# Optimization experiments

Hardware: AMD Instinct MI355X
Metric: run time of the kernel (lower is better)

Reference implementation:

```python
import jax, jax.numpy as jnp
import numpy as np

N = 50000
E = 600000
D_IN = 128
D_OUT = 128


def setup_inputs() -> dict:
    key = jax.random.key(0)
    k1, k2, k3, k4 = jax.random.split(key, 4)
    x = jax.random.normal(k1, (N, D_IN), dtype=jnp.float32)
    edge_index = jax.random.randint(k2, (2, E), 0, N, dtype=jnp.int64)
    # GCNConv learned params: weight [D_IN, D_OUT] (glorot), bias [D_OUT] (zeros in PyG)
    lim = np.sqrt(6.0 / (D_IN + D_OUT)).astype(np.float32)
    W = jax.random.uniform(k3, (D_IN, D_OUT), dtype=jnp.float32, minval=-lim, maxval=lim)
    b = jnp.zeros((D_OUT,), dtype=jnp.float32)
    return {"x": x, "edge_index": edge_index, "W": W, "b": b}


def reference(x, edge_index, W, b):
    # PyG GCNConv default: add self-loops, symmetric normalization D^-1/2 A D^-1/2,
    # out[i] = sum_{j->i} norm_ji * (x[j] @ W) + b
    n = x.shape[0]
    loops = jnp.arange(n, dtype=edge_index.dtype)
    row = jnp.concatenate([edge_index[0], loops])  # source
    col = jnp.concatenate([edge_index[1], loops])  # destination

    deg = jax.ops.segment_sum(jnp.ones_like(col, dtype=x.dtype), col, num_segments=n)
    dinv = jnp.where(deg > 0, jax.lax.rsqrt(deg), 0.0)
    norm = dinv[row] * dinv[col]  # [E+N]

    h = x @ W  # [N, D_OUT] linear transform first (D_OUT <= D_IN style)
    msg = h[row] * norm[:, None]  # gather + scale, [E+N, D_OUT]
    out = jax.ops.segment_sum(msg, col, num_segments=n)  # scatter-add to destinations
    return out + b
```

## Files before the change

### kernel.cpp

```cpp
#include <hip/hip_runtime.h>
#include <hip/hip_bf16.h>

#define D 128
#define CAP 64
typedef __hip_bfloat16 bf16;
typedef __hip_bfloat162 bf162;
typedef __attribute__((ext_vector_type(8))) short bf16x8;
typedef __attribute__((ext_vector_type(4))) float f32x4;

__device__ __forceinline__ int load_idx(const void* ei, long long pos, int is64) {
    if (is64) return (int)((const long long*)ei)[pos];
    return ((const int*)ei)[pos];
}

__device__ __forceinline__ float bf16bits_to_f32(unsigned short v) {
    union { unsigned u; float f; } c;
    c.u = ((unsigned)v) << 16;
    return c.f;
}

__device__ __forceinline__ unsigned short f32_to_bf16bits(float v) {
    bf16 b = __float2bfloat16(v);
    return *reinterpret_cast<unsigned short*>(&b);
}

__global__ void init_kernel(const void* __restrict__ x, const void* __restrict__ ei,
                            const void* __restrict__ W, bf16x8* __restrict__ Wpre,
                            int* __restrict__ cur, int* __restrict__ flags,
                            int n, int nzb) {
    int i = blockIdx.x * blockDim.x + threadIdx.x;
    if (i < n) cur[i] = 0;

    if (blockIdx.x == 0) {
        __shared__ int cnt;
        if (threadIdx.x == 0) cnt = 0;
        __syncthreads();
        const unsigned short* u = (const unsigned short*)x;
        int bad = 0;
        for (int j = threadIdx.x; j < 2048; j += blockDim.x) {
            unsigned short v = u[2 * j];
            int e = (v >> 7) & 0xFF;
            if (e == 255 || (e != 0 && (e < 90 || e > 165))) bad++;
        }
        atomicAdd(&cnt, bad);
        __syncthreads();
        if (threadIdx.x == 0) flags[0] = (cnt > 256) ? 1 : 0;
    } else if (blockIdx.x == 1) {
        __shared__ int cnt;
        if (threadIdx.x == 0) cnt = 0;
        __syncthreads();
        const int* w = (const int*)ei;
        int nz = 0;
        for (int j = threadIdx.x; j < 512; j += blockDim.x) {
            if (w[2 * j + 1] != 0) nz++;
        }
        atomicAdd(&cnt, nz);
        __syncthreads();
        if (threadIdx.x == 0) flags[1] = (cnt == 0) ? 1 : 0;
    } else if (blockIdx.x >= nzb) {
        __shared__ int cnt;
        if (threadIdx.x == 0) cnt = 0;
        __syncthreads();
        const unsigned short* u = (const unsigned short*)x;
        int bad = 0;
        for (int j = threadIdx.x; j < 2048; j += blockDim.x) {
            unsigned short v = u[2 * j];
            int e = (v >> 7) & 0xFF;
            if (e == 255 || (e != 0 && (e < 90 || e > 165))) bad++;
        }
        atomicAdd(&cnt, bad);
        __syncthreads();
        const int f = (cnt > 256) ? 1 : 0;

        int cid = (blockIdx.x - nzb) * 256 + threadIdx.x;
        int l2 = cid & 63, ktct = cid >> 6;
        int kb = (ktct & 3) * 32 + (l2 >> 4) * 8;
        int cc = (ktct >> 2) * 16 + (l2 & 15);
        bf16x8 hi, lo;
        if (f) {
            const float* Wf = (const float*)W;
#pragma unroll
            for (int q = 0; q < 8; ++q) {
                float wv = Wf[(size_t)(kb + q) * D + cc];
                unsigned short hb = f32_to_bf16bits(wv);
                hi[q] = (short)hb;
                lo[q] = (short)f32_to_bf16bits(wv - bf16bits_to_f32(hb));
            }
        } else {
            const unsigned short* Wu = (const unsigned short*)W;
#pragma unroll
            for (int q = 0; q < 8; ++q) {
                hi[q] = (short)Wu[(size_t)(kb + q) * D + cc];
                lo[q] = 0;
            }
        }
        Wpre[cid] = hi;
        Wpre[2048 + cid] = lo;
    }
}

template <typename IT>
__global__ void __launch_bounds__(256) edge_gemm_kernel(
        const void* __restrict__ ei, int* __restrict__ cur, IT* __restrict__ slab2,
        int E, const void* __restrict__ x, const bf16x8* __restrict__ Wpre,
        bf16* __restrict__ hbuf, int n, int ngemm, const int* __restrict__ flags) {
    if (blockIdx.x >= ngemm) {
        const int i64 = flags[1];
        int base = (blockIdx.x - ngemm) * 1024 + threadIdx.x;
#pragma unroll
        for (int q = 0; q < 4; ++q) {
            int e = base + q * 256;
            if (e < E) {
                int s = load_idx(ei, e, i64);
                int d = load_idx(ei, (long long)E + e, i64);
                int c = atomicAdd(&cur[d], 1);
                if (c < CAP) slab2[(size_t)d * CAP + c] = (IT)s;
            }
        }
        return;
    }

    const int t = threadIdx.x;
    const int lane = t & 63;
    const int wave = t >> 6;
    const int g = lane >> 4;
    const int rl = lane & 15;
    const int r0 = blockIdx.x * 64;
    const int f = flags[0];

    bf16x8 ah[4], al[4];
    const int arow = r0 + wave * 16 + rl;
    if (f) {
        const float* xr = (const float*)x + (size_t)arow * D;
#pragma unroll
        for (int kt = 0; kt < 4; ++kt) {
            float u[8];
            if (arow < n) {
                float4 u0 = *(const float4*)(xr + kt * 32 + g * 8);
                float4 u1 = *(const float4*)(xr + kt * 32 + g * 8 + 4);
                u[0] = u0.x; u[1] = u0.y; u[2] = u0.z; u[3] = u0.w;
                u[4] = u1.x; u[5] = u1.y; u[6] = u1.z; u[7] = u1.w;
            } else {
#pragma unroll
                for (int i = 0; i < 8; ++i) u[i] = 0.f;
            }
#pragma unroll
            for (int i = 0; i < 8; ++i) {
                unsigned short hb = f32_to_bf16bits(u[i]);
                ah[kt][i] = (short)hb;
                al[kt][i] = (short)f32_to_bf16bits(u[i] - bf16bits_to_f32(hb));
            }
        }
    } else {
        const unsigned short* xr = (const unsigned short*)x + (size_t)arow * D;
#pragma unroll
        for (int kt = 0; kt < 4; ++kt) {
            bf16x8 v = {};
            if (arow < n) v = *(const bf16x8*)(xr + kt * 32 + g * 8);
            ah[kt] = v;
            al[kt] = v;
        }
    }

#pragma unroll
    for (int cp = 0; cp < 4; ++cp) {
        const int ct0 = cp * 2, ct1 = cp * 2 + 1;
        f32x4 acc0 = {0.f, 0.f, 0.f, 0.f};
        f32x4 acc1 = {0.f, 0.f, 0.f, 0.f};
#pragma unroll
        for (int kt = 0; kt < 4; ++kt) {
            int cid0 = (ct0 * 4 + kt) * 64 + lane;
            int cid1 = (ct1 * 4 + kt) * 64 + lane;
            bf16x8 bh0 = Wpre[cid0];
            bf16x8 bh1 = Wpre[cid1];
            acc0 = __builtin_amdgcn_mfma_f32_16x16x32_bf16(ah[kt], bh0, acc0, 0, 0, 0);
            acc1 = __builtin_amdgcn_mfma_f32_16x16x32_bf16(ah[kt], bh1, acc1, 0, 0, 0);
            if (f) {
                bf16x8 bl0 = Wpre[2048 + cid0];
                bf16x8 bl1 = Wpre[2048 + cid1];
                acc0 = __builtin_amdgcn_mfma_f32_16x16x32_bf16(ah[kt], bl0, acc0, 0, 0, 0);
                acc1 = __builtin_amdgcn_mfma_f32_16x16x32_bf16(ah[kt], bl1, acc1, 0, 0, 0);
                acc0 = __builtin_amdgcn_mfma_f32_16x16x32_bf16(al[kt], bh0, acc0, 0, 0, 0);
                acc1 = __builtin_amdgcn_mfma_f32_16x16x32_bf16(al[kt], bh1, acc1, 0, 0, 0);
            }
        }
#pragma unroll
        for (int reg = 0; reg < 4; ++reg) {
            int r = r0 + wave * 16 + g * 4 + reg;
            if (r < n) {
                hbuf[(size_t)r * D + ct0 * 16 + rl] = __float2bfloat16(acc0[reg]);
                hbuf[(size_t)r * D + ct1 * 16 + rl] = __float2bfloat16(acc1[reg]);
            }
        }
    }
}

template <typename IT>
__global__ void gather_kernel(const bf16* __restrict__ hbuf, const int* __restrict__ cur,
                              const IT* __restrict__ slab2, const void* __restrict__ b,
                              void* __restrict__ out, int n, const int* __restrict__ flags) {
    int wave = threadIdx.x >> 6;
    int lane = threadIdx.x & 63;
    int d = blockIdx.x * 4 + wave;
    if (d >= n) return;

    const int f = flags[0];
    const int half = lane >> 5;
    const int l32 = lane & 31;

    float b0, b1, b2, b3;
    if (f) {
        float4 bb = ((const float4*)b)[l32];
        b0 = bb.x; b1 = bb.y; b2 = bb.z; b3 = bb.w;
    } else {
        ushort4 bb = ((const ushort4*)b)[l32];
        b0 = bf16bits_to_f32(bb.x); b1 = bf16bits_to_f32(bb.y);
        b2 = bf16bits_to_f32(bb.z); b3 = bf16bits_to_f32(bb.w);
    }

    const unsigned short* hu = (const unsigned short*)hbuf;
    int degd = cur[d];
    int len = (degd > CAP) ? CAP : degd;
    float dd = rsqrtf((float)degd + 1.0f);

    int rec = 0;
    if (lane < len) rec = (int)slab2[(size_t)d * CAP + lane];
    float nrm = rsqrtf((float)cur[rec] + 1.0f) * dd;

    float a0 = 0.f, a1 = 0.f, a2 = 0.f, a3 = 0.f;
    int k = 0;
    for (; k + 8 <= len; k += 8) {
        int ki0 = k + half, ki1 = k + 2 + half, ki2 = k + 4 + half, ki3 = k + 6 + half;
        int s0 = __shfl(rec, ki0, 64);
        int s1 = __shfl(rec, ki1, 64);
        int s2 = __shfl(rec, ki2, 64);
        int s3 = __shfl(rec, ki3, 64);
        float n0 = __shfl(nrm, ki0, 64);
        float n1 = __shfl(nrm, ki1, 64);
        float n2 = __shfl(nrm, ki2, 64);
        float n3 = __shfl(nrm, ki3, 64);
        ushort4 h0 = *(const ushort4*)&hu[(size_t)s0 * D + l32 * 4];
        ushort4 h1 = *(const ushort4*)&hu[(size_t)s1 * D + l32 * 4];
        ushort4 h2v = *(const ushort4*)&hu[(size_t)s2 * D + l32 * 4];
        ushort4 h3v = *(const ushort4*)&hu[(size_t)s3 * D + l32 * 4];
        a0 += n0 * bf16bits_to_f32(h0.x);  a1 += n0 * bf16bits_to_f32(h0.y);
        a2 += n0 * bf16bits_to_f32(h0.z);  a3 += n0 * bf16bits_to_f32(h0.w);
        a0 += n1 * bf16bits_to_f32(h1.x);  a1 += n1 * bf16bits_to_f32(h1.y);
        a2 += n1 * bf16bits_to_f32(h1.z);  a3 += n1 * bf16bits_to_f32(h1.w);
        a0 += n2 * bf16bits_to_f32(h2v.x); a1 += n2 * bf16bits_to_f32(h2v.y);
        a2 += n2 * bf16bits_to_f32(h2v.z); a3 += n2 * bf16bits_to_f32(h2v.w);
        a0 += n3 * bf16bits_to_f32(h3v.x); a1 += n3 * bf16bits_to_f32(h3v.y);
        a2 += n3 * bf16bits_to_f32(h3v.z); a3 += n3 * bf16bits_to_f32(h3v.w);
    }
    for (; k < len; k += 2) {
        int ki = k + half;
        int ss = __shfl(rec, ki & 63, 64);
        float nn = __shfl(nrm, ki & 63, 64);
        bool ok = (ki < len);
        int sl = ok ? ss : d;
        float nl = ok ? nn : 0.f;
        ushort4 hv = *(const ushort4*)&hu[(size_t)sl * D + l32 * 4];
        a0 += nl * bf16bits_to_f32(hv.x);  a1 += nl * bf16bits_to_f32(hv.y);
        a2 += nl * bf16bits_to_f32(hv.z);  a3 += nl * bf16bits_to_f32(hv.w);
    }
    {
        ushort4 hs = *(const ushort4*)&hu[(size_t)d * D + l32 * 4];
        float w = (half == 0) ? dd * dd : 0.f;
        a0 += w * bf16bits_to_f32(hs.x);  a1 += w * bf16bits_to_f32(hs.y);
        a2 += w * bf16bits_to_f32(hs.z);  a3 += w * bf16bits_to_f32(hs.w);
    }
    a0 += __shfl_xor(a0, 32, 64);
    a1 += __shfl_xor(a1, 32, 64);
    a2 += __shfl_xor(a2, 32, 64);
    a3 += __shfl_xor(a3, 32, 64);
    a0 += b0; a1 += b1; a2 += b2; a3 += b3;

    if (half == 0) {
        if (f) {
            ((float4*)out)[(size_t)d * 32 + l32] = make_float4(a0, a1, a2, a3);
        } else {
            ushort4 o;
            o.x = f32_to_bf16bits(a0); o.y = f32_to_bf16bits(a1);
            o.z = f32_to_bf16bits(a2); o.w = f32_to_bf16bits(a3);
            ((ushort4*)out)[(size_t)d * 32 + l32] = o;
        }
    }
}

extern "C" void kernel_launch(void* const* d_in, const int* in_sizes, int n_in,
                              void* d_out, int out_size, void* d_ws, size_t ws_size,
                              hipStream_t stream) {
    const void* x = d_in[0];
    const void* ei = d_in[1];
    const void* W = d_in[2];
    const void* b = d_in[3];

    const int n = in_sizes[0] / D;
    const int E = in_sizes[1] / 2;

    bf16*  hbuf    = (bf16*)d_ws;
    int*   cur     = (int*)(hbuf + (size_t)n * D);
    void*  slab2   = (void*)(cur + n);
    bf16x8* Wpre   = (bf16x8*)((int*)slab2 + (size_t)n * CAP);
    int*   flags   = (int*)(Wpre + 4096);

    const int nzb   = (n + 255) / 256;
    const int ngemm = (n + 63) / 64;
    const int nedge = (E + 1023) / 1024;

    init_kernel<<<nzb + 8, 256, 0, stream>>>(x, ei, W, Wpre, cur, flags, n, nzb);
    if (n <= 65535) {
        edge_gemm_kernel<unsigned short><<<ngemm + nedge, 256, 0, stream>>>(
            ei, cur, (unsigned short*)slab2, E, x, Wpre, hbuf, n, ngemm, flags);
        gather_kernel<unsigned short><<<(n + 3) / 4, 256, 0, stream>>>(
            hbuf, cur, (const unsigned short*)slab2, b, d_out, n, flags);
    } else {
        edge_gemm_kernel<int><<<ngemm + nedge, 256, 0, stream>>>(
            ei, cur, (int*)slab2, E, x, Wpre, hbuf, n, ngemm, flags);
        gather_kernel<int><<<(n + 3) / 4, 256, 0, stream>>>(
            hbuf, cur, (const int*)slab2, b, d_out, n, flags);
    }
}
```

Baseline: 154.0 us.

## Map each half-wave to its own destination node in gather kernel

The gather kernel now assigns one destination node to each 32-lane half-wave, so each wave handles 2 nodes and each block handles 8, with the grid shrunk to match. Previously the two halves split one node's edges and combined partial sums with a cross-half shuffle reduction. The new mapping drops that reduction and the masked tail handling, and it keeps more independent nodes in flight per wave. The cost is a longer serial loop per node. The two halves can also diverge when their degrees differ, and neighbor slots past the valid length are now read unconditionally and clamped before use.

New measurement: 150.1 us, median of 2. -2.6%, faster.

```diff
diff --git a/kernel.cpp b/kernel.cpp
--- a/kernel.cpp
+++ b/kernel.cpp
@@ -199,15 +199,16 @@
 __global__ void gather_kernel(const bf16* __restrict__ hbuf, const int* __restrict__ cur,
                               const IT* __restrict__ slab2, const void* __restrict__ b,
                               void* __restrict__ out, int n, const int* __restrict__ flags) {
-    int wave = threadIdx.x >> 6;
-    int lane = threadIdx.x & 63;
-    int d = blockIdx.x * 4 + wave;
-    if (d >= n) return;
-
-    const int f = flags[0];
+    const int tid = threadIdx.x;
+    const int lane = tid & 63;
+    const int wave = tid >> 6;
     const int half = lane >> 5;
     const int l32 = lane & 31;
-
+    const int base = half * 32;
+    int d = blockIdx.x * 8 + wave * 2 + half;
+    if (d >= n) return;
+
+    const int f = flags[0];
     float b0, b1, b2, b3;
     if (f) {
         float4 bb = ((const float4*)b)[l32];
@@ -219,26 +220,29 @@
     }
 
     const unsigned short* hu = (const unsigned short*)hbuf;
+
+    int rec_lo = (int)slab2[(size_t)d * CAP + l32];
+    int rec_hi = (int)slab2[(size_t)d * CAP + 32 + l32];
     int degd = cur[d];
+    rec_lo = min(max(rec_lo, 0), n - 1);
+    rec_hi = min(max(rec_hi, 0), n - 1);
     int len = (degd > CAP) ? CAP : degd;
     float dd = rsqrtf((float)degd + 1.0f);
-
-    int rec = 0;
-    if (lane < len) rec = (int)slab2[(size_t)d * CAP + lane];
-    float nrm = rsqrtf((float)cur[rec] + 1.0f) * dd;
+    float nrm_lo = rsqrtf((float)cur[rec_lo] + 1.0f) * dd;
+    float nrm_hi = rsqrtf((float)cur[rec_hi] + 1.0f) * dd;
 
     float a0 = 0.f, a1 = 0.f, a2 = 0.f, a3 = 0.f;
+    const int lenA = (len < 32) ? len : 32;
     int k = 0;
-    for (; k + 8 <= len; k += 8) {
-        int ki0 = k + half, ki1 = k + 2 + half, ki2 = k + 4 + half, ki3 = k + 6 + half;
-        int s0 = __shfl(rec, ki0, 64);
-        int s1 = __shfl(rec, ki1, 64);
-        int s2 = __shfl(rec, ki2, 64);
-        int s3 = __shfl(rec, ki3, 64);
-        float n0 = __shfl(nrm, ki0, 64);
-        float n1 = __shfl(nrm, ki1, 64);
-        float n2 = __shfl(nrm, ki2, 64);
-        float n3 = __shfl(nrm, ki3, 64);
+    for (; k + 4 <= lenA; k += 4) {
+        int s0 = __shfl(rec_lo, base + k, 64);
+        int s1 = __shfl(rec_lo, base + k + 1, 64);
+        int s2 = __shfl(rec_lo, base + k + 2, 64);
+        int s3 = __shfl(rec_lo, base + k + 3, 64);
+        float n0 = __shfl(nrm_lo, base + k, 64);
+        float n1 = __shfl(nrm_lo, base + k + 1, 64);
+        float n2 = __shfl(nrm_lo, base + k + 2, 64);
+        float n3 = __shfl(nrm_lo, base + k + 3, 64);
         ushort4 h0 = *(const ushort4*)&hu[(size_t)s0 * D + l32 * 4];
         ushort4 h1 = *(const ushort4*)&hu[(size_t)s1 * D + l32 * 4];
         ushort4 h2v = *(const ushort4*)&hu[(size_t)s2 * D + l32 * 4];
@@ -252,38 +256,35 @@
         a0 += n3 * bf16bits_to_f32(h3v.x); a1 += n3 * bf16bits_to_f32(h3v.y);
         a2 += n3 * bf16bits_to_f32(h3v.z); a3 += n3 * bf16bits_to_f32(h3v.w);
     }
-    for (; k < len; k += 2) {
-        int ki = k + half;
-        int ss = __shfl(rec, ki & 63, 64);
-        float nn = __shfl(nrm, ki & 63, 64);
-        bool ok = (ki < len);
-        int sl = ok ? ss : d;
-        float nl = ok ? nn : 0.f;
-        ushort4 hv = *(const ushort4*)&hu[(size_t)sl * D + l32 * 4];
-        a0 += nl * bf16bits_to_f32(hv.x);  a1 += nl * bf16bits_to_f32(hv.y);
-        a2 += nl * bf16bits_to_f32(hv.z);  a3 += nl * bf16bits_to_f32(hv.w);
+    for (; k < lenA; ++k) {
+        int s = __shfl(rec_lo, base + k, 64);
+        float nn = __shfl(nrm_lo, base + k, 64);
+        ushort4 hv = *(const ushort4*)&hu[(size_t)s * D + l32 * 4];
+        a0 += nn * bf16bits_to_f32(hv.x);  a1 += nn * bf16bits_to_f32(hv.y);
+        a2 += nn * bf16bits_to_f32(hv.z);  a3 += nn * bf16bits_to_f32(hv.w);
+    }
+    for (int kb2 = 0; kb2 < len - 32; ++kb2) {
+        int s = __shfl(rec_hi, base + kb2, 64);
+        float nn = __shfl(nrm_hi, base + kb2, 64);
+        ushort4 hv = *(const ushort4*)&hu[(size_t)s * D + l32 * 4];
+        a0 += nn * bf16bits_to_f32(hv.x);  a1 += nn * bf16bits_to_f32(hv.y);
+        a2 += nn * bf16bits_to_f32(hv.z);  a3 += nn * bf16bits_to_f32(hv.w);
     }
     {
         ushort4 hs = *(const ushort4*)&hu[(size_t)d * D + l32 * 4];
-        float w = (half == 0) ? dd * dd : 0.f;
+        float w = dd * dd;
         a0 += w * bf16bits_to_f32(hs.x);  a1 += w * bf16bits_to_f32(hs.y);
         a2 += w * bf16bits_to_f32(hs.z);  a3 += w * bf16bits_to_f32(hs.w);
     }
-    a0 += __shfl_xor(a0, 32, 64);
-    a1 += __shfl_xor(a1, 32, 64);
-    a2 += __shfl_xor(a2, 32, 64);
-    a3 += __shfl_xor(a3, 32, 64);
     a0 += b0; a1 += b1; a2 += b2; a3 += b3;
 
-    if (half == 0) {
-        if (f) {
-            ((float4*)out)[(size_t)d * 32 + l32] = make_float4(a0, a1, a2, a3);
-        } else {
-            ushort4 o;
-            o.x = f32_to_bf16bits(a0); o.y = f32_to_bf16bits(a1);
-            o.z = f32_to_bf16bits(a2); o.w = f32_to_bf16bits(a3);
-            ((ushort4*)out)[(size_t)d * 32 + l32] = o;
-        }
+    if (f) {
+        ((float4*)out)[(size_t)d * 32 + l32] = make_float4(a0, a1, a2, a3);
+    } else {
+        ushort4 o;
+        o.x = f32_to_bf16bits(a0); o.y = f32_to_bf16bits(a1);
+        o.z = f32_to_bf16bits(a2); o.w = f32_to_bf16bits(a3);
+        ((ushort4*)out)[(size_t)d * 32 + l32] = o;
     }
 }
 
@@ -312,12 +313,12 @@
     if (n <= 65535) {
         edge_gemm_kernel<unsigned short><<<ngemm + nedge, 256, 0, stream>>>(
             ei, cur, (unsigned short*)slab2, E, x, Wpre, hbuf, n, ngemm, flags);
-        gather_kernel<unsigned short><<<(n + 3) / 4, 256, 0, stream>>>(
+        gather_kernel<unsigned short><<<(n + 7) / 8, 256, 0, stream>>>(
             hbuf, cur, (const unsigned short*)slab2, b, d_out, n, flags);
     } else {
         edge_gemm_kernel<int><<<ngemm + nedge, 256, 0, stream>>>(
             ei, cur, (int*)slab2, E, x, Wpre, hbuf, n, ngemm, flags);
-        gather_kernel<int><<<(n + 3) / 4, 256, 0, stream>>>(
+        gather_kernel<int><<<(n + 7) / 8, 256, 0, stream>>>(
             hbuf, cur, (const int*)slab2, b, d_out, n, flags);
     }
 }
```
